# Performance work log

Measured on AMD Instinct MI355X. Metric: run time of the kernel, lower is better.

Reference implementation:

```python
import jax, jax.numpy as jnp
import numpy as np


def setup_inputs() -> dict:
    key = jax.random.key(0)
    ks = jax.random.split(key, 8)
    C = 512
    Cq = C // 8  # 64
    x = jax.random.normal(ks[0], (4, C, 64, 64), dtype=jnp.float32)
    # 1x1 conv == per-pixel linear; store weights as [out, in]
    Wq = jax.random.normal(ks[1], (Cq, C), dtype=jnp.float32) * (1.0 / np.sqrt(C))
    bq = jax.random.normal(ks[2], (Cq,), dtype=jnp.float32) * 0.01
    Wk = jax.random.normal(ks[3], (Cq, C), dtype=jnp.float32) * (1.0 / np.sqrt(C))
    bk = jax.random.normal(ks[4], (Cq,), dtype=jnp.float32) * 0.01
    Wv = jax.random.normal(ks[5], (C, C), dtype=jnp.float32) * (1.0 / np.sqrt(C))
    bv = jax.random.normal(ks[6], (C,), dtype=jnp.float32) * 0.01
    alpha = jax.random.normal(ks[7], (1,), dtype=jnp.float32)
    return {"x": x, "Wq": Wq, "bq": bq, "Wk": Wk, "bk": bk, "Wv": Wv, "bv": bv, "alpha": alpha}


def reference(x, Wq, bq, Wk, bk, Wv, bv, alpha):
    B, C, H, W = x.shape
    HW = H * W
    xf = x.reshape(B, C, HW)  # [B, C, HW]
    # 1x1 convs as channel matmuls
    q = jnp.einsum('oc,bcn->bon', Wq, xf) + bq[None, :, None]  # [B, Cq, HW]
    k = jnp.einsum('oc,bcn->bon', Wk, xf) + bk[None, :, None]  # [B, Cq, HW]
    v = jnp.einsum('oc,bcn->bon', Wv, xf) + bv[None, :, None]  # [B, C, HW]
    # attention[b, i, j] = softmax_j( q[:, i] . k[:, j] )
    scores = jnp.einsum('bci,bcj->bij', q, k)  # [B, HW, HW]
    attn = jax.nn.softmax(scores, axis=-1)
    # feat_e = v @ attn^T : out[b, c, i] = sum_j v[b, c, j] * attn[b, i, j]
    feat_e = jnp.einsum('bcj,bij->bci', v, attn).reshape(B, C, H, W)
    return alpha[0] * feat_e
```

## Files before the change

kernel.cpp:

```cpp
#include <hip/hip_runtime.h>
#include <hip/hip_fp16.h>

#define HW_N 4096
#define C_IN 512
#define C_Q  64
#define NB   4
#define M_Y  640
#define M_YP 768
#define LOG2E 1.4426950408889634f

typedef __attribute__((ext_vector_type(8))) short short8;
typedef __attribute__((ext_vector_type(4))) short short4v;
typedef __attribute__((ext_vector_type(4))) float float4v;
typedef unsigned short ushort_t;

__device__ __forceinline__ ushort_t f2h(float x) {
    return __half_as_ushort(__float2half(x));
}
__device__ __forceinline__ float h2f(ushort_t h) {
    return __half2float(__ushort_as_half(h));
}
__device__ __forceinline__ void gl2lds16(const ushort_t* g, ushort_t* l) {
    __builtin_amdgcn_global_load_lds(
        (const __attribute__((address_space(1))) unsigned int*)g,
        (__attribute__((address_space(3))) unsigned int*)l, 16, 0, 0);
}

__global__ __launch_bounds__(256) void split_w(const float* __restrict__ Wq,
                                               const float* __restrict__ Wk,
                                               const float* __restrict__ Wv,
                                               ushort_t* __restrict__ Wh,
                                               ushort_t* __restrict__ Wl) {
    int idx = (blockIdx.x * 256 + threadIdx.x) * 4;
#pragma unroll
    for (int e = 0; e < 4; e++) {
        int i = idx + e;
        int m = i >> 9, k = i & 511;
        float v = (m < C_Q) ? Wq[m * C_IN + k]
                 : (m < 2 * C_Q) ? Wk[(m - C_Q) * C_IN + k]
                 : (m < M_Y) ? Wv[(size_t)(m - 2 * C_Q) * C_IN + k]
                 : 0.f;
        ushort_t h = f2h(v);
        Wh[i] = h;
        Wl[i] = f2h(v - h2f(h));
    }
}

__global__ __launch_bounds__(256) void split_x(const float* __restrict__ x,
                                               ushort_t* __restrict__ xTh,
                                               ushort_t* __restrict__ xTl,
                                               float* __restrict__ D) {
    const size_t bz = blockIdx.z;
    x   += bz * ((size_t)C_IN * HW_N);
    xTh += bz * ((size_t)HW_N * C_IN);
    xTl += bz * ((size_t)HW_N * C_IN);
    D   += bz * HW_N;

    if (blockIdx.y == 0 && blockIdx.x < 16) D[blockIdx.x * 256 + threadIdx.x] = 0.f;

    __shared__ float tile[64][65];
    const int n0 = blockIdx.x * 64, k0 = blockIdx.y * 64;
    const int t = threadIdx.x;
#pragma unroll
    for (int it = 0; it < 4; it++) {
        int e = t + it * 256;
        int r = e >> 4, c4 = (e & 15) << 2;
        float4 v = *(const float4*)(x + (size_t)(k0 + r) * HW_N + n0 + c4);
        tile[r][c4 + 0] = v.x; tile[r][c4 + 1] = v.y;
        tile[r][c4 + 2] = v.z; tile[r][c4 + 3] = v.w;
    }
    __syncthreads();
    const int rr = t >> 2, kq = (t & 3) << 4;
    ushort_t h[16], l[16];
#pragma unroll
    for (int j = 0; j < 16; j++) {
        float v = tile[kq + j][rr];
        h[j] = f2h(v);
        l[j] = f2h(v - h2f(h[j]));
    }
    size_t o = (size_t)(n0 + rr) * C_IN + k0 + kq;
    *(uint4*)(xTh + o) = *(uint4*)h;
    *(uint4*)(xTh + o + 8) = *(uint4*)(h + 8);
    *(uint4*)(xTl + o) = *(uint4*)l;
    *(uint4*)(xTl + o + 8) = *(uint4*)(l + 8);
}

__global__ __launch_bounds__(512, 2) void ygemm(
    const ushort_t* __restrict__ Ah, const ushort_t* __restrict__ Al,
    const ushort_t* __restrict__ Bh, const ushort_t* __restrict__ Bl,
    const float* __restrict__ bq, const float* __restrict__ bk,
    const float* __restrict__ bv,
    ushort_t* __restrict__ qkTh, ushort_t* __restrict__ qkTl,
    ushort_t* __restrict__ Vh, ushort_t* __restrict__ Vl) {
    const size_t bz = blockIdx.z;
    Bh   += bz * ((size_t)HW_N * C_IN);
    Bl   += bz * ((size_t)HW_N * C_IN);
    qkTh += bz * ((size_t)HW_N * 2 * C_Q);
    qkTl += bz * ((size_t)HW_N * 2 * C_Q);
    Vh   += bz * ((size_t)C_IN * HW_N);
    Vl   += bz * ((size_t)C_IN * HW_N);

    __shared__ ushort_t sAh[2][256 * 32];
    __shared__ ushort_t sAl[2][256 * 32];
    __shared__ ushort_t sBh[2][256 * 32];
    __shared__ ushort_t sBl[2][256 * 32];

    const int tid = threadIdx.x, w = tid >> 6, lane = tid & 63;
    const int quad = lane >> 4, lr = lane & 15;
    const int m0 = blockIdx.y * 256, n0 = blockIdx.x * 256;

    const int mat = w >> 1, half = w & 1;
    const ushort_t* src;
    ushort_t* dst0;
    int rowBase;
    if (mat == 0)      { src = Ah; dst0 = sAh[0]; rowBase = m0; }
    else if (mat == 1) { src = Al; dst0 = sAl[0]; rowBase = m0; }
    else if (mat == 2) { src = Bh; dst0 = sBh[0]; rowBase = n0; }
    else               { src = Bl; dst0 = sBl[0]; rowBase = n0; }
    const int cr = lane >> 2, uv = lane & 3;
    const int kcol = (uv ^ ((cr >> 1) & 3)) << 3;
    const ushort_t* gk = src + (size_t)(rowBase + half * 128 + cr) * C_IN + kcol;
    const int cOfs = half * 8;

    const int wm = (w & 3) * 64, wn = (w >> 2) * 128;
    const int up = (quad ^ ((lr >> 1) & 3)) << 3;

    float4v acc[4][8];
#pragma unroll
    for (int i = 0; i < 4; i++)
#pragma unroll
        for (int j = 0; j < 8; j++) acc[i][j] = (float4v){0.f, 0.f, 0.f, 0.f};

#pragma unroll
    for (int c = 0; c < 8; c++)
        gl2lds16(gk + (size_t)(c * 16) * C_IN, dst0 + (cOfs + c) * 512);
    __syncthreads();

    const int NSTEP = C_IN / 32;
    for (int it = 0; it < NSTEP; ++it) {
        const int cur = it & 1, nxt = cur ^ 1;

        if (it + 1 < NSTEP) {
            ushort_t* db = dst0 + nxt * (256 * 32);
#pragma unroll
            for (int c = 0; c < 8; c++)
                gl2lds16(gk + (size_t)(c * 16) * C_IN + (it + 1) * 32,
                         db + (cOfs + c) * 512);
        }

        short8 bh[8], bl[8];
#pragma unroll
        for (int j = 0; j < 8; j++) {
            const int row = wn + j * 16 + lr;
            bh[j] = *(const short8*)&sBh[cur][row * 32 + up];
            bl[j] = *(const short8*)&sBl[cur][row * 32 + up];
        }
#pragma unroll
        for (int i = 0; i < 4; i++) {
            const int row = wm + i * 16 + lr;
            short8 ah = *(const short8*)&sAh[cur][row * 32 + up];
            short8 al = *(const short8*)&sAl[cur][row * 32 + up];
#pragma unroll
            for (int j = 0; j < 8; j++)
                acc[i][j] = __builtin_amdgcn_mfma_f32_16x16x32_f16(ah, bh[j], acc[i][j], 0, 0, 0);
#pragma unroll
            for (int j = 0; j < 8; j++)
                acc[i][j] = __builtin_amdgcn_mfma_f32_16x16x32_f16(ah, bl[j], acc[i][j], 0, 0, 0);
#pragma unroll
            for (int j = 0; j < 8; j++)
                acc[i][j] = __builtin_amdgcn_mfma_f32_16x16x32_f16(al, bh[j], acc[i][j], 0, 0, 0);
        }
        __syncthreads();
    }

#pragma unroll
    for (int i = 0; i < 4; i++)
#pragma unroll
        for (int j = 0; j < 8; j++)
#pragma unroll
            for (int r = 0; r < 4; r++) {
                const int m = m0 + wm + i * 16 + quad * 4 + r;
                if (m >= M_Y) continue;
                const int n = n0 + wn + j * 16 + lr;
                float bi = (m < C_Q) ? bq[m]
                          : (m < 2 * C_Q) ? bk[m - C_Q] : bv[m - 2 * C_Q];
                float v = acc[i][j][r] + bi;
                ushort_t h = f2h(v);
                ushort_t lo = f2h(v - h2f(h));
                if (m < 2 * C_Q) {
                    qkTh[(size_t)n * (2 * C_Q) + m] = h;
                    qkTl[(size_t)n * (2 * C_Q) + m] = lo;
                } else {
                    Vh[(size_t)(m - 2 * C_Q) * HW_N + n] = h;
                    Vl[(size_t)(m - 2 * C_Q) * HW_N + n] = lo;
                }
            }
}

__global__ __launch_bounds__(512, 2) void qkgemm(const ushort_t* __restrict__ qkTh_,
                                                 const ushort_t* __restrict__ qkTl_,
                                                 float* __restrict__ outF,
                                                 float* __restrict__ Dsum) {
    __shared__ ushort_t sAh[2][256 * 32];
    __shared__ ushort_t sAl[2][256 * 32];
    __shared__ ushort_t sBh[2][256 * 32];
    __shared__ ushort_t sBl[2][256 * 32];

    const int tid = threadIdx.x, w = tid >> 6, lane = tid & 63;
    const int quad = lane >> 4, lr = lane & 15;
    const int m0 = blockIdx.y * 256, n0 = blockIdx.x * 256;

    const int mat = w >> 1, ks = w & 1;
    const ushort_t* src = ((mat & 1) ? qkTl_ : qkTh_) + ((mat >> 1) ? C_Q : 0);
    ushort_t* dst0 = ((mat == 0) ? sAh : (mat == 1) ? sAl
                    : (mat == 2) ? sBh : sBl)[ks];
    const int rowBase = (mat >> 1) ? n0 : m0;
    const int cr = lane >> 2, uv = lane & 3;
    const int kcol = (uv ^ ((cr >> 1) & 3)) << 3;
    const ushort_t* gk = src + (size_t)(rowBase + cr) * (2 * C_Q) + ks * 32 + kcol;

    const int wm = (w & 3) * 64, wn = (w >> 2) * 128;
    const int up = (quad ^ ((lr >> 1) & 3)) << 3;

#pragma unroll
    for (int c = 0; c < 16; c++)
        gl2lds16(gk + (size_t)(c * 16) * (2 * C_Q), dst0 + c * 512);

    float4v acc[4][8];
#pragma unroll
    for (int i = 0; i < 4; i++)
#pragma unroll
        for (int j = 0; j < 8; j++) acc[i][j] = (float4v){0.f, 0.f, 0.f, 0.f};

    __syncthreads();

#pragma unroll
    for (int k2 = 0; k2 < 2; k2++) {
        short8 bh[8], bl[8];
#pragma unroll
        for (int j = 0; j < 8; j++) {
            const int row = wn + j * 16 + lr;
            bh[j] = *(const short8*)&sBh[k2][row * 32 + up];
            bl[j] = *(const short8*)&sBl[k2][row * 32 + up];
        }
#pragma unroll
        for (int i = 0; i < 4; i++) {
            const int row = wm + i * 16 + lr;
            short8 ah = *(const short8*)&sAh[k2][row * 32 + up];
            short8 al = *(const short8*)&sAl[k2][row * 32 + up];
#pragma unroll
            for (int j = 0; j < 8; j++)
                acc[i][j] = __builtin_amdgcn_mfma_f32_16x16x32_f16(ah, bh[j], acc[i][j], 0, 0, 0);
#pragma unroll
            for (int j = 0; j < 8; j++)
                acc[i][j] = __builtin_amdgcn_mfma_f32_16x16x32_f16(ah, bl[j], acc[i][j], 0, 0, 0);
#pragma unroll
            for (int j = 0; j < 8; j++)
                acc[i][j] = __builtin_amdgcn_mfma_f32_16x16x32_f16(al, bh[j], acc[i][j], 0, 0, 0);
        }
    }

#pragma unroll
    for (int i = 0; i < 4; i++) {
#pragma unroll
        for (int r = 0; r < 4; r++) {
            float s = 0.f;
#pragma unroll
            for (int j = 0; j < 8; j++) {
                const int m = m0 + wm + i * 16 + quad * 4 + r;
                const int n = n0 + wn + j * 16 + lr;
                outF[(size_t)m * HW_N + n] = acc[i][j][r];
                s += __expf(acc[i][j][r]);
            }
            s += __shfl_xor(s, 1);
            s += __shfl_xor(s, 2);
            s += __shfl_xor(s, 4);
            s += __shfl_xor(s, 8);
            if (lr == 0)
                atomicAdd(&Dsum[m0 + wm + i * 16 + quad * 4 + r], s);
        }
    }
}

__global__ __launch_bounds__(512, 2) void feat7(const ushort_t* __restrict__ Vh,
                                                const ushort_t* __restrict__ Vl,
                                                const float* __restrict__ S,
                                                const float* __restrict__ D,
                                                float* __restrict__ out,
                                                float* __restrict__ part,
                                                int kLen) {
    __shared__ ushort_t sVh[2][256 * 32];
    __shared__ ushort_t sVl[2][256 * 32];
    __shared__ ushort_t sP [2][256 * 32];

    const int tid = threadIdx.x, w = tid >> 6, lane = tid & 63;
    const int quad = lane >> 4, lr = lane & 15;
    const int m0 = blockIdx.y * 256, n0 = blockIdx.x * 256;
    const int k0 = blockIdx.z * kLen;

    const int crv = lane >> 2, uv = lane & 3;
    const int vcol = (uv ^ ((crv >> 1) & 3)) << 3;
    const ushort_t* vbase = (w < 4) ? Vh : Vl;
    const ushort_t* gVsrc[4];
    int sOfs[4];
#pragma unroll
    for (int c = 0; c < 4; c++) {
        const int chunk = ((w & 3) * 4 + c);
        gVsrc[c] = vbase + (size_t)(m0 + chunk * 16 + crv) * HW_N + vcol + k0;
        sOfs[c] = chunk * 512;
    }

    const int pr = tid >> 3, pu = tid & 7;
    const float* gS = S + (size_t)(n0 + pr) * HW_N + k0 + pu * 4;
    const int pdst = (((pu >> 1) ^ ((pr >> 1) & 3)) << 3) + ((pu & 1) << 2);
    float lrw[4];
#pragma unroll
    for (int c = 0; c < 4; c++) lrw[c] = -log2f(D[n0 + pr + 64 * c]);

    const int wm = (w & 3) * 64, wn = (w >> 2) * 128;

    float4 sreg[4];
    const int nIter = kLen >> 5;

    {
#pragma unroll
        for (int c = 0; c < 4; c++)
            sreg[c] = *(const float4*)(gS + (size_t)(64 * c) * HW_N);
#pragma unroll
        for (int c = 0; c < 4; c++) gl2lds16(gVsrc[c], ((w < 4) ? sVh : sVl)[0] + sOfs[c]);
#pragma unroll
        for (int c = 0; c < 4; c++) {
            ushort_t h4[4];
            h4[0] = f2h(exp2f(fmaf(sreg[c].x, LOG2E, lrw[c])));
            h4[1] = f2h(exp2f(fmaf(sreg[c].y, LOG2E, lrw[c])));
            h4[2] = f2h(exp2f(fmaf(sreg[c].z, LOG2E, lrw[c])));
            h4[3] = f2h(exp2f(fmaf(sreg[c].w, LOG2E, lrw[c])));
            *(short4v*)&sP[0][(pr + 64 * c) * 32 + pdst] = *(short4v*)h4;
        }
        if (nIter > 1) {
#pragma unroll
            for (int c = 0; c < 4; c++)
                sreg[c] = *(const float4*)(gS + (size_t)(64 * c) * HW_N + 32);
        }
    }
    __syncthreads();

    float4v acc[4][8];
#pragma unroll
    for (int i = 0; i < 4; i++)
#pragma unroll
        for (int j = 0; j < 8; j++) acc[i][j] = (float4v){0.f, 0.f, 0.f, 0.f};

    for (int it = 0; it < nIter; ++it) {
        const int kk = it << 5;
        const int cur = it & 1, nxt = cur ^ 1;

        if (it + 1 < nIter) {
            ushort_t* db = ((w < 4) ? sVh : sVl)[nxt];
#pragma unroll
            for (int c = 0; c < 4; c++) gl2lds16(gVsrc[c] + kk + 32, db + sOfs[c]);
        }

        short8 bh[8];
#pragma unroll
        for (int j = 0; j < 8; j++) {
            const int row = wn + j * 16 + lr;
            bh[j] = *(const short8*)&sP[cur][row * 32 + ((quad ^ ((lr >> 1) & 3)) << 3)];
        }

        if (it + 1 < nIter) {
#pragma unroll
            for (int c = 0; c < 4; c++) {
                ushort_t h4[4];
                h4[0] = f2h(exp2f(fmaf(sreg[c].x, LOG2E, lrw[c])));
                h4[1] = f2h(exp2f(fmaf(sreg[c].y, LOG2E, lrw[c])));
                h4[2] = f2h(exp2f(fmaf(sreg[c].z, LOG2E, lrw[c])));
                h4[3] = f2h(exp2f(fmaf(sreg[c].w, LOG2E, lrw[c])));
                *(short4v*)&sP[nxt][(pr + 64 * c) * 32 + pdst] = *(short4v*)h4;
            }
            if (it + 2 < nIter) {
#pragma unroll
                for (int c = 0; c < 4; c++)
                    sreg[c] = *(const float4*)(gS + (size_t)(64 * c) * HW_N + kk + 64);
            }
        }

#pragma unroll
        for (int i = 0; i < 4; i++) {
            const int row = wm + i * 16 + lr;
            const int up = (quad ^ ((lr >> 1) & 3)) << 3;
            short8 ah = *(const short8*)&sVh[cur][row * 32 + up];
            short8 al = *(const short8*)&sVl[cur][row * 32 + up];
#pragma unroll
            for (int j = 0; j < 8; j++)
                acc[i][j] = __builtin_amdgcn_mfma_f32_16x16x32_f16(ah, bh[j], acc[i][j], 0, 0, 0);
#pragma unroll
            for (int j = 0; j < 8; j++)
                acc[i][j] = __builtin_amdgcn_mfma_f32_16x16x32_f16(al, bh[j], acc[i][j], 0, 0, 0);
        }
        __syncthreads();
    }

    float* o = (blockIdx.z == 0) ? out
             : (part + (size_t)(blockIdx.z - 1) * ((size_t)C_IN * HW_N));
#pragma unroll
    for (int i = 0; i < 4; i++)
#pragma unroll
        for (int j = 0; j < 8; j++)
#pragma unroll
            for (int r = 0; r < 4; r++) {
                const int m = m0 + wm + i * 16 + quad * 4 + r;
                const int n = n0 + wn + j * 16 + lr;
                o[(size_t)m * HW_N + n] = acc[i][j][r];
            }
}

__global__ __launch_bounds__(256) void reduce_alphaN(float* __restrict__ out,
                                                     const float4* __restrict__ part,
                                                     size_t stride4,
                                                     const float* __restrict__ alpha,
                                                     int np) {
    const size_t i = (size_t)blockIdx.x * 256 + threadIdx.x;
    const float a = alpha[0];
    float4* out4 = (float4*)out;
    float4 s = out4[i];
    for (int p = 0; p < np; p++) {
        float4 t = part[i + (size_t)p * stride4];
        s.x += t.x; s.y += t.y; s.z += t.z; s.w += t.w;
    }
    float4 o;
    o.x = a * s.x; o.y = a * s.y; o.z = a * s.z; o.w = a * s.w;
    out4[i] = o;
}


extern "C" void kernel_launch(void* const* d_in, const int* in_sizes, int n_in,
                              void* d_out, int out_size, void* d_ws, size_t ws_size,
                              hipStream_t stream) {
    const float* x     = (const float*)d_in[0];
    const float* Wq    = (const float*)d_in[1];
    const float* bq    = (const float*)d_in[2];
    const float* Wk    = (const float*)d_in[3];
    const float* bk    = (const float*)d_in[4];
    const float* Wv    = (const float*)d_in[5];
    const float* bv    = (const float*)d_in[6];
    const float* alpha = (const float*)d_in[7];
    float* out = (float*)d_out;

    const size_t planeQK = (size_t)HW_N * 2 * C_Q;
    const size_t planeV  = (size_t)C_IN * HW_N;
    const size_t planeXT = (size_t)HW_N * C_IN;
    const size_t planeW  = (size_t)M_YP * C_IN;
    const size_t planeS  = (size_t)HW_N * HW_N;

    const size_t fusedBytes =
        (size_t)NB * HW_N * 4 + 2 * (size_t)NB * planeQK * 2 +
        2 * (size_t)NB * planeV * 2 + 2 * planeW * 2 + planeS * 4 +
        7 * planeV * 4;
    const bool fused = (ws_size >= fusedBytes);

    if (fused) {
        float* D4      = (float*)d_ws;
        ushort_t* qkTh4 = (ushort_t*)(D4 + (size_t)NB * HW_N);
        ushort_t* qkTl4 = qkTh4 + (size_t)NB * planeQK;
        ushort_t* Vh4   = qkTl4 + (size_t)NB * planeQK;
        ushort_t* Vl4   = Vh4 + (size_t)NB * planeV;
        ushort_t* Wh    = Vl4 + (size_t)NB * planeV;
        ushort_t* Wl    = Wh + planeW;
        float* scores   = (float*)(Wl + planeW);
        float* part     = scores + planeS;
        ushort_t* xTh4  = (ushort_t*)scores;
        ushort_t* xTl4  = xTh4 + (size_t)NB * planeXT;

        split_w<<<dim3(M_YP * C_IN / 4 / 256), dim3(256), 0, stream>>>(Wq, Wk, Wv, Wh, Wl);

        split_x<<<dim3(HW_N / 64, C_IN / 64, NB), dim3(256), 0, stream>>>(
            x, xTh4, xTl4, D4);
        ygemm<<<dim3(HW_N / 256, M_YP / 256, NB), dim3(512), 0, stream>>>(
            Wh, Wl, xTh4, xTl4, bq, bk, bv, qkTh4, qkTl4, Vh4, Vl4);

        for (int b = 0; b < NB; b++) {
            float* outb = out + (size_t)b * planeV;
            qkgemm<<<dim3(HW_N / 256, HW_N / 256), dim3(512), 0, stream>>>(
                qkTh4 + (size_t)b * planeQK, qkTl4 + (size_t)b * planeQK,
                scores, D4 + (size_t)b * HW_N);
            feat7<<<dim3(HW_N / 256, C_IN / 256, 8), dim3(512), 0, stream>>>(
                Vh4 + (size_t)b * planeV, Vl4 + (size_t)b * planeV,
                scores, D4 + (size_t)b * HW_N, outb, part, HW_N / 8);
            reduce_alphaN<<<dim3((C_IN * HW_N / 4) / 256), dim3(256), 0, stream>>>(
                outb, (const float4*)part, planeV / 4, alpha, 7);
        }
        return;
    }

    float* D = (float*)d_ws;
    ushort_t* qkTh = (ushort_t*)(D + HW_N);
    ushort_t* qkTl = qkTh + planeQK;
    ushort_t* Vh   = qkTl + planeQK;
    ushort_t* Vl   = Vh + planeV;
    ushort_t* Wh   = Vl + planeV;
    ushort_t* Wl   = Wh + planeW;
    float* scores  = (float*)(Wl + planeW);
    float* part    = scores + planeS;
    ushort_t* xTh  = (ushort_t*)scores;
    ushort_t* xTl  = xTh + planeXT;

    const size_t baseF = (size_t)(part - (float*)d_ws);
    const int zsplit = (ws_size >= (baseF + 7 * planeV) * sizeof(float)) ? 8 : 4;

    split_w<<<dim3(M_YP * C_IN / 4 / 256), dim3(256), 0, stream>>>(Wq, Wk, Wv, Wh, Wl);

    for (int b = 0; b < NB; b++) {
        const float* xb = x + (size_t)b * planeV;
        float* outb = out + (size_t)b * planeV;

        split_x<<<dim3(HW_N / 64, C_IN / 64, 1), dim3(256), 0, stream>>>(
            xb, xTh, xTl, D);
        ygemm<<<dim3(HW_N / 256, M_YP / 256, 1), dim3(512), 0, stream>>>(
            Wh, Wl, xTh, xTl, bq, bk, bv, qkTh, qkTl, Vh, Vl);
        qkgemm<<<dim3(HW_N / 256, HW_N / 256), dim3(512), 0, stream>>>(
            qkTh, qkTl, scores, D);
        feat7<<<dim3(HW_N / 256, C_IN / 256, zsplit), dim3(512), 0, stream>>>(
            Vh, Vl, scores, D, outb, part, HW_N / zsplit);
        reduce_alphaN<<<dim3((C_IN * HW_N / 4) / 256), dim3(256), 0, stream>>>(
            outb, (const float4*)part, planeV / 4, alpha, zsplit - 1);
    }
}
```

Before: 471.5 us.

## Replace split-K partial buffers and reduce kernel with atomic accumulation into output

The feature kernel now folds alpha into the fp16 probability values and accumulates its split-K partial results directly into the output with float atomics. The separate reduce kernel and its seven partial planes are removed, and one kernel zeroes the output up front. The goal is to drop the round trip through the partial buffers and one launch per batch. In exchange it adds atomic traffic, makes the summation order nondeterministic, and scaling probabilities by alpha before the fp16 conversion may change precision.

```diff
diff --git a/kernel.cpp b/kernel.cpp
--- a/kernel.cpp
+++ b/kernel.cpp
@@ -44,6 +44,11 @@
         Wh[i] = h;
         Wl[i] = f2h(v - h2f(h));
     }
+}
+
+__global__ __launch_bounds__(256) void zero_out(float4* __restrict__ p, int n4) {
+    int i = blockIdx.x * 256 + threadIdx.x;
+    if (i < n4) p[i] = (float4){0.f, 0.f, 0.f, 0.f};
 }
 
 __global__ __launch_bounds__(256) void split_x(const float* __restrict__ x,
@@ -282,12 +287,12 @@
     }
 }
 
-__global__ __launch_bounds__(512, 2) void feat7(const ushort_t* __restrict__ Vh,
+__global__ __launch_bounds__(512, 2) void feat8(const ushort_t* __restrict__ Vh,
                                                 const ushort_t* __restrict__ Vl,
                                                 const float* __restrict__ S,
                                                 const float* __restrict__ D,
                                                 float* __restrict__ out,
-                                                float* __restrict__ part,
+                                                const float* __restrict__ alpha,
                                                 int kLen) {
     __shared__ ushort_t sVh[2][256 * 32];
     __shared__ ushort_t sVl[2][256 * 32];
@@ -297,6 +302,7 @@
     const int quad = lane >> 4, lr = lane & 15;
     const int m0 = blockIdx.y * 256, n0 = blockIdx.x * 256;
     const int k0 = blockIdx.z * kLen;
+    const float a = alpha[0];
 
     const int crv = lane >> 2, uv = lane & 3;
     const int vcol = (uv ^ ((crv >> 1) & 3)) << 3;
@@ -331,10 +337,10 @@
 #pragma unroll
         for (int c = 0; c < 4; c++) {
             ushort_t h4[4];
-            h4[0] = f2h(exp2f(fmaf(sreg[c].x, LOG2E, lrw[c])));
-            h4[1] = f2h(exp2f(fmaf(sreg[c].y, LOG2E, lrw[c])));
-            h4[2] = f2h(exp2f(fmaf(sreg[c].z, LOG2E, lrw[c])));
-            h4[3] = f2h(exp2f(fmaf(sreg[c].w, LOG2E, lrw[c])));
+            h4[0] = f2h(a * exp2f(fmaf(sreg[c].x, LOG2E, lrw[c])));
+            h4[1] = f2h(a * exp2f(fmaf(sreg[c].y, LOG2E, lrw[c])));
+            h4[2] = f2h(a * exp2f(fmaf(sreg[c].z, LOG2E, lrw[c])));
+            h4[3] = f2h(a * exp2f(fmaf(sreg[c].w, LOG2E, lrw[c])));
             *(short4v*)&sP[0][(pr + 64 * c) * 32 + pdst] = *(short4v*)h4;
         }
         if (nIter > 1) {
@@ -372,10 +378,10 @@
 #pragma unroll
             for (int c = 0; c < 4; c++) {
                 ushort_t h4[4];
-                h4[0] = f2h(exp2f(fmaf(sreg[c].x, LOG2E, lrw[c])));
-                h4[1] = f2h(exp2f(fmaf(sreg[c].y, LOG2E, lrw[c])));
-                h4[2] = f2h(exp2f(fmaf(sreg[c].z, LOG2E, lrw[c])));
-                h4[3] = f2h(exp2f(fmaf(sreg[c].w, LOG2E, lrw[c])));
+                h4[0] = f2h(a * exp2f(fmaf(sreg[c].x, LOG2E, lrw[c])));
+                h4[1] = f2h(a * exp2f(fmaf(sreg[c].y, LOG2E, lrw[c])));
+                h4[2] = f2h(a * exp2f(fmaf(sreg[c].z, LOG2E, lrw[c])));
+                h4[3] = f2h(a * exp2f(fmaf(sreg[c].w, LOG2E, lrw[c])));
                 *(short4v*)&sP[nxt][(pr + 64 * c) * 32 + pdst] = *(short4v*)h4;
             }
             if (it + 2 < nIter) {
@@ -401,8 +407,6 @@
         __syncthreads();
     }
 
-    float* o = (blockIdx.z == 0) ? out
-             : (part + (size_t)(blockIdx.z - 1) * ((size_t)C_IN * HW_N));
 #pragma unroll
     for (int i = 0; i < 4; i++)
 #pragma unroll
@@ -411,26 +415,8 @@
             for (int r = 0; r < 4; r++) {
                 const int m = m0 + wm + i * 16 + quad * 4 + r;
                 const int n = n0 + wn + j * 16 + lr;
-                o[(size_t)m * HW_N + n] = acc[i][j][r];
+                unsafeAtomicAdd(&out[(size_t)m * HW_N + n], acc[i][j][r]);
             }
-}
-
-__global__ __launch_bounds__(256) void reduce_alphaN(float* __restrict__ out,
-                                                     const float4* __restrict__ part,
-                                                     size_t stride4,
-                                                     const float* __restrict__ alpha,
-                                                     int np) {
-    const size_t i = (size_t)blockIdx.x * 256 + threadIdx.x;
-    const float a = alpha[0];
-    float4* out4 = (float4*)out;
-    float4 s = out4[i];
-    for (int p = 0; p < np; p++) {
-        float4 t = part[i + (size_t)p * stride4];
-        s.x += t.x; s.y += t.y; s.z += t.z; s.w += t.w;
-    }
-    float4 o;
-    o.x = a * s.x; o.y = a * s.y; o.z = a * s.z; o.w = a * s.w;
-    out4[i] = o;
 }
 
 
@@ -455,9 +441,10 @@
 
     const size_t fusedBytes =
         (size_t)NB * HW_N * 4 + 2 * (size_t)NB * planeQK * 2 +
-        2 * (size_t)NB * planeV * 2 + 2 * planeW * 2 + planeS * 4 +
-        7 * planeV * 4;
+        2 * (size_t)NB * planeV * 2 + 2 * planeW * 2 + planeS * 4;
     const bool fused = (ws_size >= fusedBytes);
+
+    const int nOut4 = (int)((size_t)NB * planeV / 4);
 
     if (fused) {
         float* D4      = (float*)d_ws;
@@ -468,11 +455,12 @@
         ushort_t* Wh    = Vl4 + (size_t)NB * planeV;
         ushort_t* Wl    = Wh + planeW;
         float* scores   = (float*)(Wl + planeW);
-        float* part     = scores + planeS;
         ushort_t* xTh4  = (ushort_t*)scores;
         ushort_t* xTl4  = xTh4 + (size_t)NB * planeXT;
 
         split_w<<<dim3(M_YP * C_IN / 4 / 256), dim3(256), 0, stream>>>(Wq, Wk, Wv, Wh, Wl);
+        zero_out<<<dim3((nOut4 + 255) / 256), dim3(256), 0, stream>>>(
+            (float4*)out, nOut4);
 
         split_x<<<dim3(HW_N / 64, C_IN / 64, NB), dim3(256), 0, stream>>>(
             x, xTh4, xTl4, D4);
@@ -484,11 +472,9 @@
             qkgemm<<<dim3(HW_N / 256, HW_N / 256), dim3(512), 0, stream>>>(
                 qkTh4 + (size_t)b * planeQK, qkTl4 + (size_t)b * planeQK,
                 scores, D4 + (size_t)b * HW_N);
-            feat7<<<dim3(HW_N / 256, C_IN / 256, 8), dim3(512), 0, stream>>>(
+            feat8<<<dim3(HW_N / 256, C_IN / 256, 8), dim3(512), 0, stream>>>(
                 Vh4 + (size_t)b * planeV, Vl4 + (size_t)b * planeV,
-                scores, D4 + (size_t)b * HW_N, outb, part, HW_N / 8);
-            reduce_alphaN<<<dim3((C_IN * HW_N / 4) / 256), dim3(256), 0, stream>>>(
-                outb, (const float4*)part, planeV / 4, alpha, 7);
+                scores, D4 + (size_t)b * HW_N, outb, alpha, HW_N / 8);
         }
         return;
     }
@@ -501,14 +487,12 @@
     ushort_t* Wh   = Vl + planeV;
     ushort_t* Wl   = Wh + planeW;
     float* scores  = (float*)(Wl + planeW);
-    float* part    = scores + planeS;
     ushort_t* xTh  = (ushort_t*)scores;
     ushort_t* xTl  = xTh + planeXT;
 
-    const size_t baseF = (size_t)(part - (float*)d_ws);
-    const int zsplit = (ws_size >= (baseF + 7 * planeV) * sizeof(float)) ? 8 : 4;
-
     split_w<<<dim3(M_YP * C_IN / 4 / 256), dim3(256), 0, stream>>>(Wq, Wk, Wv, Wh, Wl);
+    zero_out<<<dim3((nOut4 + 255) / 256), dim3(256), 0, stream>>>(
+        (float4*)out, nOut4);
 
     for (int b = 0; b < NB; b++) {
         const float* xb = x + (size_t)b * planeV;
@@ -520,9 +504,7 @@
             Wh, Wl, xTh, xTl, bq, bk, bv, qkTh, qkTl, Vh, Vl);
         qkgemm<<<dim3(HW_N / 256, HW_N / 256), dim3(512), 0, stream>>>(
             qkTh, qkTl, scores, D);
-        feat7<<<dim3(HW_N / 256, C_IN / 256, zsplit), dim3(512), 0, stream>>>(
-            Vh, Vl, scores, D, outb, part, HW_N / zsplit);
-        reduce_alphaN<<<dim3((C_IN * HW_N / 4) / 256), dim3(256), 0, stream>>>(
-            outb, (const float4*)part, planeV / 4, alpha, zsplit - 1);
-    }
-}
+        feat8<<<dim3(HW_N / 256, C_IN / 256, 8), dim3(512), 0, stream>>>(
+            Vh, Vl, scores, D, outb, alpha, HW_N / 8);
+    }
+}
```

After: 590.1 us. +25.2%, slower.
